# Kernel tuning notes

Hardware: AMD Instinct MI355X
Metric: run time of the kernel (lower is better)

## Reference

```python
import jax, jax.numpy as jnp
import numpy as np

# Water box constants: n_atoms=192 -> 64 oxygens (type 8) + 128 hydrogens (type 1)
N_O, N_H = 64, 128
XLIM = 6.0  # params.max_rdf_dist


def _hist(d, bins):
    """np.histogram-equivalent fixed-bin histogram of 1-D values d."""
    nb = bins.shape[0] - 1
    idx = jnp.clip(jnp.searchsorted(bins, d, side='right') - 1, 0, nb - 1)
    w = ((d >= bins[0]) & (d <= bins[-1])).astype(jnp.float32)
    return jnp.zeros((nb,), jnp.float32).at[idx].add(w)


def _pair_rdf(wrapped, idx0, idx1, lattices, bins):
    # wrapped: [T, N, 3]; replicates distance_pbc_select + histogram/RDF math
    x0 = wrapped[:, idx0]                       # [T, n0, 3] (type1 atoms)
    x1 = wrapped[:, idx1]                       # [T, n1, 3] (type2 atoms)
    # x0.repeat([1,n1,1]) vs x1.repeat_interleave(n0) == outer pairing (x1 outer, x0 inner)
    delta = jnp.abs(x0[:, None, :, :] - x1[:, :, None, :])   # [T, n1, n0, 3]
    delta = jnp.where(delta > 0.5 * lattices, delta - lattices, delta)
    s = (delta ** 2).sum(-1)                    # [T, n1, n0]
    # safe sqrt (self-pairs give exact zeros)
    d = jnp.where(s > 0, jnp.sqrt(jnp.where(s > 0, s, 1.0)), 0.0)
    T = d.shape[0]
    P = d.shape[1] * d.shape[2]
    d = d.reshape(T, P)
    hists = jax.vmap(lambda dd: _hist(dd, bins))(d)          # [T, nb]
    vol = jnp.prod(lattices)
    shell = (4.0 / 3.0) * jnp.pi * (bins[1:] ** 3 - bins[:-1] ** 3)
    # aggregate RDF over all frames (zeros fall below bins[0]=1e-6, excluded)
    Z1 = (T * P / vol) * shell
    data_rdf = hists.sum(0) / Z1
    # per-frame RDFs, renormalized to the aggregate RDF's total mass
    Z2 = (T / vol) * shell
    rdfs = hists / Z2
    rdfs = rdfs / rdfs.sum(1, keepdims=True) * data_rdf.sum()
    return rdfs.mean(0)                          # [nb]


def setup_inputs() -> dict:
    key = jax.random.key(0)
    k0, k1, k2, k3 = jax.random.split(key, 4)
    T, R, N, nb = 100, 8, 192, 600
    stacked_radii = jax.random.normal(k0, (T, R, N, 3), jnp.float32) * 5.0
    ptypes = jnp.tile(jnp.array([8, 1, 1], jnp.int32), N // 3)  # O,H,H per water
    lattices = jnp.full((3,), 12.42, jnp.float32)
    bins = jnp.asarray(np.linspace(1e-6, XLIM, nb + 1), jnp.float32)
    gt_oo = jax.random.uniform(k1, (1, nb), jnp.float32)
    gt_hh = jax.random.uniform(k2, (1, nb), jnp.float32)
    gt_ho = jax.random.uniform(k3, (1, nb), jnp.float32)
    return dict(stacked_radii=stacked_radii, ptypes=ptypes, lattices=lattices,
                bins=bins, gt_oo=gt_oo, gt_hh=gt_hh, gt_ho=gt_ho)


def reference(stacked_radii, ptypes, lattices, bins, gt_oo, gt_hh, gt_ho):
    idx_O = jnp.nonzero(ptypes == 8, size=N_O)[0]
    idx_H = jnp.nonzero(ptypes == 1, size=N_H)[0]

    def per_replica(data):                       # data: [T, N, 3]
        wrapped = data / lattices % 1 * lattices  # PBC wrap into box
        rdf_oo = _pair_rdf(wrapped, idx_O, idx_O, lattices, bins)
        rdf_hh = _pair_rdf(wrapped, idx_H, idx_H, lattices, bins)
        rdf_ho = _pair_rdf(wrapped, idx_H, idx_O, lattices, bins)
        maes = jnp.stack([
            XLIM * jnp.abs(rdf_oo[None] - gt_oo).mean(),
            XLIM * jnp.abs(rdf_hh[None] - gt_hh).mean(),
            XLIM * jnp.abs(rdf_ho[None] - gt_ho).mean(),
        ])
        return jnp.concatenate([rdf_oo, rdf_hh, rdf_ho]), maes.max()

    # [T, R, N, 3] -> [R, T, N, 3], vmap over replicas
    rdf_list, max_maes = jax.vmap(per_replica)(jnp.swapaxes(stacked_radii, 0, 1))
    return rdf_list, max_maes
```

## Files before the change

### kernel.cpp

```cpp
#include <hip/hip_runtime.h>

#define T_STEPS 100
#define R_REP   8
#define N_ATOMS 192
#define NBINS   600

__global__ __launch_bounds__(256) void rdf_hist_kernel(
    const float* __restrict__ radii,
    const float* __restrict__ lattices,
    const float* __restrict__ bins,
    float* __restrict__ hist_out,
    float* __restrict__ sigma_out)
{
#pragma clang fp contract(off)
    __shared__ float    Tq[NBINS + 2];
    __shared__ unsigned shist[4][NBINS];
    __shared__ float4   sA[128];
    __shared__ float4   sB[64];
    __shared__ float    sred[256];

    const int blk = blockIdx.x;
    const int p   = blk % 3;
    const int t   = (blk / 3) % T_STEPS;
    const int r   = blk / (3 * T_STEPS);
    const int tid = threadIdx.x;

    for (int b = tid; b <= NBINS + 1; b += 256) {
        if (b <= NBINS) {
            float e = bins[b];
            unsigned u = __float_as_uint(e * e);
            while (sqrtf(__uint_as_float(u)) <  e) ++u;
            while (sqrtf(__uint_as_float(u - 1)) >= e) --u;
            Tq[b] = __uint_as_float(u);
        } else {
            unsigned u = __float_as_uint(36.0f);
            while (sqrtf(__uint_as_float(u)) <= 6.0f) ++u;
            while (sqrtf(__uint_as_float(u - 1)) > 6.0f) --u;
            Tq[NBINS + 1] = __uint_as_float(u);
        }
    }
    for (int b = tid; b < NBINS; b += 256) {
        shist[0][b] = 0u; shist[1][b] = 0u; shist[2][b] = 0u; shist[3][b] = 0u;
    }

    const float L0 = lattices[0], L1 = lattices[1], L2 = lattices[2];
    const float* base = radii + (size_t)(t * R_REP + r) * (N_ATOMS * 3);

    auto load_set = [&](float4* dst, int n, bool isH) {
#pragma clang fp contract(off)
        for (int a = tid; a < n; a += 256) {
            int atom = isH ? (3 * (a >> 1) + 1 + (a & 1)) : (3 * a);
            const float* src = base + atom * 3;
            float x = src[0], y = src[1], z = src[2];
            float qx = x / L0; float wx = (qx - floorf(qx)) * L0;
            float qy = y / L1; float wy = (qy - floorf(qy)) * L1;
            float qz = z / L2; float wz = (qz - floorf(qz)) * L2;
            dst[a] = make_float4(wx, wy, wz, 0.0f);
        }
    };

    if (p == 0)      { load_set(sA, 64, false); }
    else if (p == 1) { load_set(sA, 128, true); }
    else             { load_set(sA, 128, true); load_set(sB, 64, false); }
    __syncthreads();

    const float T0 = Tq[0];
    const float TG = Tq[NBINS + 1];
    const float b0f = bins[0];
    const float invstep = (float)NBINS / (6.0f - b0f);
    const float h0 = 0.5f * L0, h1 = 0.5f * L1, h2 = 0.5f * L2;
    unsigned* myh = shist[tid >> 6];

    auto bin_pair = [&](float4 A, float4 B, unsigned w) {
#pragma clang fp contract(off)
        float dx = fabsf(A.x - B.x); dx = fminf(dx, fabsf(dx - L0));
        float dy = fabsf(A.y - B.y); dy = fminf(dy, fabsf(dy - L1));
        float dz = fabsf(A.z - B.z); dz = fminf(dz, fabsf(dz - L2));
        float s = dx * dx + dy * dy + dz * dz;
        if (s < T0 || s >= TG) return;
        float dhat = __builtin_amdgcn_sqrtf(s);
        int k0 = (int)((dhat - b0f) * invstep);
        if (k0 > NBINS - 1) k0 = NBINS - 1;
        float lo = Tq[k0], hi = Tq[k0 + 1];
        int bi = k0 + (int)(s >= hi) - (int)(s < lo);
        if (bi > NBINS - 1) bi = NBINS - 1;
        atomicAdd(&myh[bi], w);
    };

    if (p == 2) {
        float4 A = sA[tid & 127];
        int jbase = (tid >> 7);
#pragma unroll
        for (int it = 0; it < 32; ++it)
            bin_pair(A, sB[jbase + it * 2], 1u);
    } else if (p == 1) {
        int i = tid & 127;
        float4 A = sA[i];
        int kbase = (tid >> 7) + 1;
#pragma unroll
        for (int it = 0; it < 32; ++it) {
            int k = kbase + it * 2;
            bin_pair(A, sA[(i + k) & 127], (k == 64) ? 1u : 2u);
        }
    } else {
        int i = tid & 63;
        float4 A = sA[i];
        int kbase = (tid >> 6) + 1;
#pragma unroll
        for (int it = 0; it < 8; ++it) {
            int k = kbase + it * 4;
            bin_pair(A, sA[(i + k) & 63], (k == 32) ? 1u : 2u);
        }
    }
    __syncthreads();

    float* outp = hist_out + (size_t)((r * 3 + p) * T_STEPS + t) * NBINS;
    float lsig = 0.0f;
    for (int b = tid; b < NBINS; b += 256) {
        float fc = (float)(shist[0][b] + shist[1][b] + shist[2][b] + shist[3][b]);
        outp[b] = fc;
        float e0 = bins[b], e1 = bins[b + 1];
        float shell = 4.18879020478639053f * (e1 * e1 * e1 - e0 * e0 * e0);
        lsig += fc / shell;
    }
    sred[tid] = lsig;
    __syncthreads();
    for (int s2 = 128; s2 > 0; s2 >>= 1) {
        if (tid < s2) sred[tid] += sred[tid + s2];
        __syncthreads();
    }
    if (tid == 0) sigma_out[(r * 3 + p) * T_STEPS + t] = sred[0];
}

__global__ __launch_bounds__(640) void rdf_norm_kernel(
    const float* __restrict__ hist,
    const float* __restrict__ sigma,
    const float* __restrict__ bins,
    const float* __restrict__ lattices,
    const float* __restrict__ gt_oo,
    const float* __restrict__ gt_hh,
    const float* __restrict__ gt_ho,
    float* __restrict__ out)
{
#pragma clang fp contract(off)
    __shared__ float ssig[T_STEPS];
    __shared__ float sinvsig[T_STEPS];
    __shared__ float sred[640];
    __shared__ float sS;

    const int blk = blockIdx.x;
    const int p = blk % 3, r = blk / 3;
    const int tid = threadIdx.x;
    const float* h = hist + (size_t)blk * T_STEPS * NBINS;

    if (tid < T_STEPS) {
        float sg = sigma[blk * T_STEPS + tid];
        ssig[tid] = sg;
        sinvsig[tid] = 1.0f / sg;
    }
    __syncthreads();
    if (tid == 0) {
        float s = 0.0f;
        for (int t = 0; t < T_STEPS; ++t) s += ssig[t];
        float vol = lattices[0] * lattices[1] * lattices[2];
        float Pf = (p == 0) ? 4096.0f : ((p == 1) ? 16384.0f : 8192.0f);
        sS = vol / ((float)T_STEPS * Pf) * s;
    }
    __syncthreads();

    const float S = sS;
    const float* gt = (p == 0) ? gt_oo : ((p == 1) ? gt_hh : gt_ho);
    float lacc = 0.0f;
    const int b = tid;
    if (b < NBINS) {
        float a0 = 0.0f, a1 = 0.0f, a2 = 0.0f, a3 = 0.0f;
        const float* hb = h + b;
        for (int t = 0; t < T_STEPS; t += 4) {
            a0 += hb[(t + 0) * NBINS] * sinvsig[t + 0];
            a1 += hb[(t + 1) * NBINS] * sinvsig[t + 1];
            a2 += hb[(t + 2) * NBINS] * sinvsig[t + 2];
            a3 += hb[(t + 3) * NBINS] * sinvsig[t + 3];
        }
        float e0 = bins[b], e1 = bins[b + 1];
        float shell = 4.18879020478639053f * (e1 * e1 * e1 - e0 * e0 * e0);
        float v = S * (1.0f / (float)T_STEPS) * (1.0f / shell) * ((a0 + a1) + (a2 + a3));
        out[r * 1800 + p * 600 + b] = v;
        lacc = fabsf(v - gt[b]);
    }
    sred[tid] = lacc;
    __syncthreads();
    for (int s2 = 512; s2 > 0; s2 >>= 1) {
        if (tid < s2 && tid + s2 < 640) sred[tid] += sred[tid + s2];
        __syncthreads();
    }
    if (tid == 0) {
        float mae = 6.0f * (sred[0] / 600.0f);
        atomicMax((int*)&out[14400 + r], __float_as_int(mae));
    }
}

extern "C" void kernel_launch(void* const* d_in, const int* in_sizes, int n_in,
                              void* d_out, int out_size, void* d_ws, size_t ws_size,
                              hipStream_t stream) {
    const float* radii    = (const float*)d_in[0];
    const float* lattices = (const float*)d_in[2];
    const float* bins     = (const float*)d_in[3];
    const float* gt_oo    = (const float*)d_in[4];
    const float* gt_hh    = (const float*)d_in[5];
    const float* gt_ho    = (const float*)d_in[6];
    float* out = (float*)d_out;

    float* hist  = (float*)d_ws;
    float* sigma = hist + (size_t)R_REP * 3 * T_STEPS * NBINS;

    hipLaunchKernelGGL(rdf_hist_kernel, dim3(R_REP * 3 * T_STEPS), dim3(256), 0, stream,
                       radii, lattices, bins, hist, sigma);
    hipLaunchKernelGGL(rdf_norm_kernel, dim3(R_REP * 3), dim3(640), 0, stream,
                       hist, sigma, bins, lattices, gt_oo, gt_hh, gt_ho, out);
}
```

Before: 92.53 us.

## Fuse three pair types into one block per frame and use wave-shuffle reductions

```diff
diff --git a/kernel.cpp b/kernel.cpp
--- a/kernel.cpp
+++ b/kernel.cpp
@@ -14,15 +14,13 @@
 {
 #pragma clang fp contract(off)
     __shared__ float    Tq[NBINS + 2];
-    __shared__ unsigned shist[4][NBINS];
-    __shared__ float4   sA[128];
-    __shared__ float4   sB[64];
-    __shared__ float    sred[256];
+    __shared__ unsigned shist[2][3][NBINS];
+    __shared__ float4   sAtom[192];
+    __shared__ float    spart[4][3];
 
     const int blk = blockIdx.x;
-    const int p   = blk % 3;
-    const int t   = (blk / 3) % T_STEPS;
-    const int r   = blk / (3 * T_STEPS);
+    const int t   = blk % T_STEPS;
+    const int r   = blk / T_STEPS;
     const int tid = threadIdx.x;
 
     for (int b = tid; b <= NBINS + 1; b += 256) {
@@ -40,38 +38,33 @@
         }
     }
     for (int b = tid; b < NBINS; b += 256) {
-        shist[0][b] = 0u; shist[1][b] = 0u; shist[2][b] = 0u; shist[3][b] = 0u;
+        shist[0][0][b] = 0u; shist[0][1][b] = 0u; shist[0][2][b] = 0u;
+        shist[1][0][b] = 0u; shist[1][1][b] = 0u; shist[1][2][b] = 0u;
     }
 
     const float L0 = lattices[0], L1 = lattices[1], L2 = lattices[2];
     const float* base = radii + (size_t)(t * R_REP + r) * (N_ATOMS * 3);
 
-    auto load_set = [&](float4* dst, int n, bool isH) {
-#pragma clang fp contract(off)
-        for (int a = tid; a < n; a += 256) {
-            int atom = isH ? (3 * (a >> 1) + 1 + (a & 1)) : (3 * a);
-            const float* src = base + atom * 3;
-            float x = src[0], y = src[1], z = src[2];
-            float qx = x / L0; float wx = (qx - floorf(qx)) * L0;
-            float qy = y / L1; float wy = (qy - floorf(qy)) * L1;
-            float qz = z / L2; float wz = (qz - floorf(qz)) * L2;
-            dst[a] = make_float4(wx, wy, wz, 0.0f);
-        }
-    };
-
-    if (p == 0)      { load_set(sA, 64, false); }
-    else if (p == 1) { load_set(sA, 128, true); }
-    else             { load_set(sA, 128, true); load_set(sB, 64, false); }
+    for (int a = tid; a < 192; a += 256) {
+        int atom = (a < 64) ? (3 * a)
+                            : (3 * ((a - 64) >> 1) + 1 + ((a - 64) & 1));
+        const float* src = base + atom * 3;
+        float x = src[0], y = src[1], z = src[2];
+        float qx = x / L0; float wx = (qx - floorf(qx)) * L0;
+        float qy = y / L1; float wy = (qy - floorf(qy)) * L1;
+        float qz = z / L2; float wz = (qz - floorf(qz)) * L2;
+        sAtom[a] = make_float4(wx, wy, wz, 0.0f);
+    }
     __syncthreads();
 
     const float T0 = Tq[0];
     const float TG = Tq[NBINS + 1];
     const float b0f = bins[0];
     const float invstep = (float)NBINS / (6.0f - b0f);
-    const float h0 = 0.5f * L0, h1 = 0.5f * L1, h2 = 0.5f * L2;
-    unsigned* myh = shist[tid >> 6];
-
-    auto bin_pair = [&](float4 A, float4 B, unsigned w) {
+    const int bank = tid >> 7;
+
+    auto bin_pair = [&](const float4& A, const float4& B, unsigned w,
+                        unsigned* myh) {
 #pragma clang fp contract(off)
         float dx = fabsf(A.x - B.x); dx = fminf(dx, fabsf(dx - L0));
         float dy = fabsf(A.y - B.y); dy = fminf(dy, fabsf(dy - L1));
@@ -87,49 +80,68 @@
         atomicAdd(&myh[bi], w);
     };
 
-    if (p == 2) {
-        float4 A = sA[tid & 127];
-        int jbase = (tid >> 7);
+    {
+        int i = tid & 63;
+        float4 A = sAtom[i];
+        int kbase = (tid >> 6) + 1;
+        unsigned* myh = shist[bank][0];
 #pragma unroll
-        for (int it = 0; it < 32; ++it)
-            bin_pair(A, sB[jbase + it * 2], 1u);
-    } else if (p == 1) {
+        for (int it = 0; it < 8; ++it) {
+            int k = kbase + it * 4;
+            bin_pair(A, sAtom[(i + k) & 63], (k == 32) ? 1u : 2u, myh);
+        }
+    }
+    {
         int i = tid & 127;
-        float4 A = sA[i];
+        float4 A = sAtom[64 + i];
         int kbase = (tid >> 7) + 1;
+        unsigned* myh = shist[bank][1];
 #pragma unroll
         for (int it = 0; it < 32; ++it) {
             int k = kbase + it * 2;
-            bin_pair(A, sA[(i + k) & 127], (k == 64) ? 1u : 2u);
-        }
-    } else {
-        int i = tid & 63;
-        float4 A = sA[i];
-        int kbase = (tid >> 6) + 1;
+            bin_pair(A, sAtom[64 + ((i + k) & 127)], (k == 64) ? 1u : 2u, myh);
+        }
+    }
+    {
+        int i = tid & 127;
+        float4 A = sAtom[64 + i];
+        int jbase = tid >> 7;
+        unsigned* myh = shist[bank][2];
 #pragma unroll
-        for (int it = 0; it < 8; ++it) {
-            int k = kbase + it * 4;
-            bin_pair(A, sA[(i + k) & 63], (k == 32) ? 1u : 2u);
-        }
-    }
-    __syncthreads();
-
-    float* outp = hist_out + (size_t)((r * 3 + p) * T_STEPS + t) * NBINS;
-    float lsig = 0.0f;
+        for (int it = 0; it < 32; ++it)
+            bin_pair(A, sAtom[jbase + it * 2], 1u, myh);
+    }
+    __syncthreads();
+
+    float lsig0 = 0.0f, lsig1 = 0.0f, lsig2 = 0.0f;
+    float* outp = hist_out + ((size_t)(r * 3) * T_STEPS + t) * NBINS;
     for (int b = tid; b < NBINS; b += 256) {
-        float fc = (float)(shist[0][b] + shist[1][b] + shist[2][b] + shist[3][b]);
-        outp[b] = fc;
         float e0 = bins[b], e1 = bins[b + 1];
         float shell = 4.18879020478639053f * (e1 * e1 * e1 - e0 * e0 * e0);
-        lsig += fc / shell;
-    }
-    sred[tid] = lsig;
-    __syncthreads();
-    for (int s2 = 128; s2 > 0; s2 >>= 1) {
-        if (tid < s2) sred[tid] += sred[tid + s2];
-        __syncthreads();
-    }
-    if (tid == 0) sigma_out[(r * 3 + p) * T_STEPS + t] = sred[0];
+        float f0 = (float)(shist[0][0][b] + shist[1][0][b]);
+        float f1 = (float)(shist[0][1][b] + shist[1][1][b]);
+        float f2 = (float)(shist[0][2][b] + shist[1][2][b]);
+        outp[b] = f0;
+        outp[(size_t)T_STEPS * NBINS + b] = f1;
+        outp[(size_t)(2 * T_STEPS) * NBINS + b] = f2;
+        lsig0 += f0 / shell;
+        lsig1 += f1 / shell;
+        lsig2 += f2 / shell;
+    }
+    for (int off = 32; off > 0; off >>= 1) {
+        lsig0 += __shfl_down(lsig0, off);
+        lsig1 += __shfl_down(lsig1, off);
+        lsig2 += __shfl_down(lsig2, off);
+    }
+    const int wid = tid >> 6, lane = tid & 63;
+    if (lane == 0) {
+        spart[wid][0] = lsig0; spart[wid][1] = lsig1; spart[wid][2] = lsig2;
+    }
+    __syncthreads();
+    if (tid < 3) {
+        float s = spart[0][tid] + spart[1][tid] + spart[2][tid] + spart[3][tid];
+        sigma_out[(r * 3 + tid) * T_STEPS + t] = s;
+    }
 }
 
 __global__ __launch_bounds__(640) void rdf_norm_kernel(
@@ -145,7 +157,7 @@
 #pragma clang fp contract(off)
     __shared__ float ssig[T_STEPS];
     __shared__ float sinvsig[T_STEPS];
-    __shared__ float sred[640];
+    __shared__ float swred[10];
     __shared__ float sS;
 
     const int blk = blockIdx.x;
@@ -187,14 +199,15 @@
         out[r * 1800 + p * 600 + b] = v;
         lacc = fabsf(v - gt[b]);
     }
-    sred[tid] = lacc;
-    __syncthreads();
-    for (int s2 = 512; s2 > 0; s2 >>= 1) {
-        if (tid < s2 && tid + s2 < 640) sred[tid] += sred[tid + s2];
-        __syncthreads();
-    }
+    for (int off = 32; off > 0; off >>= 1)
+        lacc += __shfl_down(lacc, off);
+    const int wid = tid >> 6, lane = tid & 63;
+    if (lane == 0) swred[wid] = lacc;
+    __syncthreads();
     if (tid == 0) {
-        float mae = 6.0f * (sred[0] / 600.0f);
+        float s = 0.0f;
+        for (int w = 0; w < 10; ++w) s += swred[w];
+        float mae = 6.0f * (s / 600.0f);
         atomicMax((int*)&out[14400 + r], __float_as_int(mae));
     }
 }
@@ -213,7 +226,7 @@
     float* hist  = (float*)d_ws;
     float* sigma = hist + (size_t)R_REP * 3 * T_STEPS * NBINS;
 
-    hipLaunchKernelGGL(rdf_hist_kernel, dim3(R_REP * 3 * T_STEPS), dim3(256), 0, stream,
+    hipLaunchKernelGGL(rdf_hist_kernel, dim3(R_REP * T_STEPS), dim3(256), 0, stream,
                        radii, lattices, bins, hist, sigma);
     hipLaunchKernelGGL(rdf_norm_kernel, dim3(R_REP * 3), dim3(640), 0, stream,
                        hist, sigma, bins, lattices, gt_oo, gt_hh, gt_ho, out);
```

After: 92.88 us. No clear change (+0.4%).
